# Performance work log

Hardware: AMD Instinct MI355X
Metric: run time of the kernel (lower is better)

The kernel has to match this reference:

```python
import jax, jax.numpy as jnp
import numpy as np

L, B, D = 4096, 4, 1024

def setup_inputs() -> dict:
    key = jax.random.key(0)
    k1, k2, k3, k4 = jax.random.split(key, 4)
    return {
        "x": jax.random.normal(k1, (L, B, D), dtype=jnp.float32),
        "lmlg": jax.random.normal(k2, (D,), dtype=jnp.float32),
        "theta": jax.random.normal(k3, (D,), dtype=jnp.float32),
        "last_conv_init": jax.random.normal(k4, (D,), dtype=jnp.float32),
    }

def reference(x, lmlg, theta, last_conv_init):
    seq_len, batch, dim = x.shape
    # per-channel decay*rotation: c = gamma * e^{i*theta}, gamma = exp(-exp(lmlg))
    gamma = jnp.exp(-jnp.exp(lmlg))                       # [D]
    c = gamma * jnp.exp(1j * theta)                       # [D] complex64
    # causal filter c^n for n = 0..L-1
    n = jnp.arange(seq_len)[:, None]                      # [L,1]
    filt = c[None, :] ** n                                # [L,D] complex64
    # linear (causal) convolution via zero-padded FFT of length 2L
    filt_fft = jnp.fft.fft(filt, n=2 * seq_len, axis=0)   # [2L,D]
    x_fft = jnp.fft.fft(x, n=2 * seq_len, axis=0)         # [2L,B,D]
    conv_filter_x = jnp.fft.ifft(filt_fft[:, None, :] * x_fft, axis=0)[:seq_len]  # [L,B,D]
    # carry-in state (fresh state = last_conv_init expanded; detached in torch)
    last_conv = jax.lax.stop_gradient(
        jnp.broadcast_to(last_conv_init.astype(conv_filter_x.dtype), (batch, dim))
    )                                                     # [B,D]
    conv_with_past = conv_filter_x + last_conv[None, :, :] * filt[:, None, :] * c[None, None, :]
    return conv_with_past.real * x
```

## Files before the change

### kernel.cpp

```cpp
#include <hip/hip_runtime.h>


#define L_  4096
#define B_  4
#define D_  1024
#define BD_ (B_ * D_)

__global__ __launch_bounds__(256) void sc_sum(
    const float* __restrict__ x,
    const float* __restrict__ lmlg,
    const float* __restrict__ theta,
    float2* __restrict__ ws, int ch) {
  const int t  = threadIdx.x;
  const int k  = blockIdx.x / B_;
  const int b  = blockIdx.x % B_;
  const int d0 = t * 4;

  float4 lg = *(const float4*)(lmlg + d0);
  float4 th = *(const float4*)(theta + d0);
  float cr[4], ci[4], sr[4] = {0.f,0.f,0.f,0.f}, si[4] = {0.f,0.f,0.f,0.f};
  {
    float g0 = expf(-expf(lg.x)), g1 = expf(-expf(lg.y));
    float g2 = expf(-expf(lg.z)), g3 = expf(-expf(lg.w));
    cr[0] = g0 * cosf(th.x); ci[0] = g0 * sinf(th.x);
    cr[1] = g1 * cosf(th.y); ci[1] = g1 * sinf(th.y);
    cr[2] = g2 * cosf(th.z); ci[2] = g2 * sinf(th.z);
    cr[3] = g3 * cosf(th.w); ci[3] = g3 * sinf(th.w);
  }

  const float* xp = x + (size_t)k * ch * BD_ + (size_t)b * D_ + d0;
#pragma unroll 4
  for (int j = 0; j < ch; ++j) {
    float4 xv = *(const float4*)(xp + (size_t)j * BD_);
    float xa[4] = {xv.x, xv.y, xv.z, xv.w};
#pragma unroll
    for (int q = 0; q < 4; ++q) {
      float nr = fmaf(cr[q], sr[q], fmaf(-ci[q], si[q], xa[q]));
      float ni = fmaf(cr[q], si[q], ci[q] * sr[q]);
      sr[q] = nr; si[q] = ni;
    }
  }

  float2* wp = ws + (size_t)(k * B_ + b) * D_ + d0;
  wp[0] = make_float2(sr[0], si[0]);
  wp[1] = make_float2(sr[1], si[1]);
  wp[2] = make_float2(sr[2], si[2]);
  wp[3] = make_float2(sr[3], si[3]);
}

__global__ __launch_bounds__(256) void sc_out(
    const float* __restrict__ x,
    const float* __restrict__ lmlg,
    const float* __restrict__ theta,
    const float* __restrict__ init,
    const float2* __restrict__ ws,
    float* __restrict__ out, int ch) {
  const int t  = threadIdx.x;
  const int k  = blockIdx.x / B_;
  const int b  = blockIdx.x % B_;
  const int d0 = t * 4;

  float4 lg = *(const float4*)(lmlg + d0);
  float4 th = *(const float4*)(theta + d0);
  float cr[4], ci[4];
  {
    float g0 = expf(-expf(lg.x)), g1 = expf(-expf(lg.y));
    float g2 = expf(-expf(lg.z)), g3 = expf(-expf(lg.w));
    cr[0] = g0 * cosf(th.x); ci[0] = g0 * sinf(th.x);
    cr[1] = g1 * cosf(th.y); ci[1] = g1 * sinf(th.y);
    cr[2] = g2 * cosf(th.z); ci[2] = g2 * sinf(th.z);
    cr[3] = g3 * cosf(th.w); ci[3] = g3 * sinf(th.w);
  }

  const float chf = (float)ch;
  float Cr[4], Ci[4];
  {
    float e0 = expf(lg.x), e1 = expf(lg.y), e2 = expf(lg.z), e3 = expf(lg.w);
    float g0 = expf(-e0 * chf), g1 = expf(-e1 * chf);
    float g2 = expf(-e2 * chf), g3 = expf(-e3 * chf);
    Cr[0] = g0 * cosf(th.x * chf); Ci[0] = g0 * sinf(th.x * chf);
    Cr[1] = g1 * cosf(th.y * chf); Ci[1] = g1 * sinf(th.y * chf);
    Cr[2] = g2 * cosf(th.z * chf); Ci[2] = g2 * sinf(th.z * chf);
    Cr[3] = g3 * cosf(th.w * chf); Ci[3] = g3 * sinf(th.w * chf);
  }

  float4 iv = *(const float4*)(init + d0);
  float hr[4] = {iv.x, iv.y, iv.z, iv.w};
  float hi[4] = {0.f, 0.f, 0.f, 0.f};
  for (int kk = 0; kk < k; ++kk) {
    const float2* sp = ws + (size_t)(kk * B_ + b) * D_ + d0;
    float2 s0 = sp[0], s1 = sp[1], s2 = sp[2], s3 = sp[3];
    float sxr[4] = {s0.x, s1.x, s2.x, s3.x};
    float sxi[4] = {s0.y, s1.y, s2.y, s3.y};
#pragma unroll
    for (int q = 0; q < 4; ++q) {
      float nr = fmaf(Cr[q], hr[q], fmaf(-Ci[q], hi[q], sxr[q]));
      float ni = fmaf(Cr[q], hi[q], fmaf(Ci[q], hr[q], sxi[q]));
      hr[q] = nr; hi[q] = ni;
    }
  }

  const size_t off = (size_t)k * ch * BD_ + (size_t)b * D_ + d0;
  const float* xp = x + off;
  float*       op = out + off;
#pragma unroll 4
  for (int j = 0; j < ch; ++j) {
    float4 xv = *(const float4*)(xp + (size_t)j * BD_);
    float xa[4] = {xv.x, xv.y, xv.z, xv.w};
    float4 res; float* ra = &res.x;
#pragma unroll
    for (int q = 0; q < 4; ++q) {
      float nr = fmaf(cr[q], hr[q], fmaf(-ci[q], hi[q], xa[q]));
      float ni = fmaf(cr[q], hi[q], ci[q] * hr[q]);
      hr[q] = nr; hi[q] = ni;
      ra[q] = nr * xa[q];
    }
    *(float4*)(op + (size_t)j * BD_) = res;
  }
}

__global__ __launch_bounds__(256) void sc_full(
    const float* __restrict__ x, const float* __restrict__ lmlg,
    const float* __restrict__ theta, const float* __restrict__ init,
    float* __restrict__ out) {
  const int idx = blockIdx.x * 256 + threadIdx.x;
  const int d   = idx & (D_ - 1);
  float g = expf(-expf(lmlg[d]));
  float cr = g * cosf(theta[d]), ci = g * sinf(theta[d]);
  float hr = init[d], hi = 0.f;
  const float* xp = x + idx;
  float*       op = out + idx;
  for (int n = 0; n < L_; ++n) {
    float xv = xp[(size_t)n * BD_];
    float nr = fmaf(cr, hr, fmaf(-ci, hi, xv));
    float ni = fmaf(cr, hi, ci * hr);
    hr = nr; hi = ni;
    op[(size_t)n * BD_] = nr * xv;
  }
}

extern "C" void kernel_launch(void* const* d_in, const int* in_sizes, int n_in,
                              void* d_out, int out_size, void* d_ws, size_t ws_size,
                              hipStream_t stream) {
  const float* x     = (const float*)d_in[0];
  const float* lmlg  = (const float*)d_in[1];
  const float* theta = (const float*)d_in[2];
  const float* init  = (const float*)d_in[3];
  float*  out = (float*)d_out;
  float2* ws  = (float2*)d_ws;

  const size_t row_bytes = (size_t)BD_ * sizeof(float2);
  int nc = 128;
  while (nc > 1 && (size_t)nc * row_bytes > ws_size) nc >>= 1;

  if (nc >= 2 && (size_t)nc * row_bytes <= ws_size) {
    const int ch = L_ / nc;
    sc_sum<<<nc * B_, 256, 0, stream>>>(x, lmlg, theta, ws, ch);
    sc_out<<<nc * B_, 256, 0, stream>>>(x, lmlg, theta, init, ws, out, ch);
  } else {
    sc_full<<<BD_ / 256, 256, 0, stream>>>(x, lmlg, theta, init, out);
  }
}
```

Before: 148.9 us.

## Fuse chunked scan into single decoupled-lookback kernel with register-cached inputs

After: 361.7 us. 2.43x slower.

```diff
diff --git a/kernel.cpp b/kernel.cpp
--- a/kernel.cpp
+++ b/kernel.cpp
@@ -5,117 +5,152 @@
 #define B_  4
 #define D_  1024
 #define BD_ (B_ * D_)
-
-__global__ __launch_bounds__(256) void sc_sum(
-    const float* __restrict__ x,
-    const float* __restrict__ lmlg,
-    const float* __restrict__ theta,
-    float2* __restrict__ ws, int ch) {
-  const int t  = threadIdx.x;
-  const int k  = blockIdx.x / B_;
-  const int b  = blockIdx.x % B_;
-  const int d0 = t * 4;
-
-  float4 lg = *(const float4*)(lmlg + d0);
-  float4 th = *(const float4*)(theta + d0);
-  float cr[4], ci[4], sr[4] = {0.f,0.f,0.f,0.f}, si[4] = {0.f,0.f,0.f,0.f};
-  {
-    float g0 = expf(-expf(lg.x)), g1 = expf(-expf(lg.y));
-    float g2 = expf(-expf(lg.z)), g3 = expf(-expf(lg.w));
-    cr[0] = g0 * cosf(th.x); ci[0] = g0 * sinf(th.x);
-    cr[1] = g1 * cosf(th.y); ci[1] = g1 * sinf(th.y);
-    cr[2] = g2 * cosf(th.z); ci[2] = g2 * sinf(th.z);
-    cr[3] = g3 * cosf(th.w); ci[3] = g3 * sinf(th.w);
-  }
-
-  const float* xp = x + (size_t)k * ch * BD_ + (size_t)b * D_ + d0;
-#pragma unroll 4
-  for (int j = 0; j < ch; ++j) {
-    float4 xv = *(const float4*)(xp + (size_t)j * BD_);
-    float xa[4] = {xv.x, xv.y, xv.z, xv.w};
-#pragma unroll
-    for (int q = 0; q < 4; ++q) {
-      float nr = fmaf(cr[q], sr[q], fmaf(-ci[q], si[q], xa[q]));
-      float ni = fmaf(cr[q], si[q], ci[q] * sr[q]);
-      sr[q] = nr; si[q] = ni;
-    }
-  }
-
-  float2* wp = ws + (size_t)(k * B_ + b) * D_ + d0;
-  wp[0] = make_float2(sr[0], si[0]);
-  wp[1] = make_float2(sr[1], si[1]);
-  wp[2] = make_float2(sr[2], si[2]);
-  wp[3] = make_float2(sr[3], si[3]);
-}
-
-__global__ __launch_bounds__(256) void sc_out(
+#define NC  128
+#define CH  32
+
+
+__global__ __launch_bounds__(256, 2) void sc_lookback(
     const float* __restrict__ x,
     const float* __restrict__ lmlg,
     const float* __restrict__ theta,
     const float* __restrict__ init,
-    const float2* __restrict__ ws,
-    float* __restrict__ out, int ch) {
-  const int t  = threadIdx.x;
-  const int k  = blockIdx.x / B_;
-  const int b  = blockIdx.x % B_;
-  const int d0 = t * 4;
+    float* __restrict__ out,
+    float2* __restrict__ agg,
+    float2* __restrict__ inc,
+    unsigned int* __restrict__ flags) {
+  const int t    = threadIdx.x;
+  const int k    = blockIdx.x / B_;
+  const int b    = blockIdx.x % B_;
+  const int d0   = t * 4;
+  const int lane = t & 63;
 
   float4 lg = *(const float4*)(lmlg + d0);
   float4 th = *(const float4*)(theta + d0);
-  float cr[4], ci[4];
+  float cr[4], ci[4], Cr[4], Ci[4];
   {
-    float g0 = expf(-expf(lg.x)), g1 = expf(-expf(lg.y));
-    float g2 = expf(-expf(lg.z)), g3 = expf(-expf(lg.w));
-    cr[0] = g0 * cosf(th.x); ci[0] = g0 * sinf(th.x);
-    cr[1] = g1 * cosf(th.y); ci[1] = g1 * sinf(th.y);
-    cr[2] = g2 * cosf(th.z); ci[2] = g2 * sinf(th.z);
-    cr[3] = g3 * cosf(th.w); ci[3] = g3 * sinf(th.w);
-  }
-
-  const float chf = (float)ch;
-  float Cr[4], Ci[4];
+    float e[4] = {expf(lg.x), expf(lg.y), expf(lg.z), expf(lg.w)};
+    float ta[4] = {th.x, th.y, th.z, th.w};
+#pragma unroll
+    for (int c = 0; c < 4; ++c) {
+      float g = expf(-e[c]);
+      cr[c] = g * cosf(ta[c]);  ci[c] = g * sinf(ta[c]);
+      float gC = expf(-e[c] * (float)CH);
+      Cr[c] = gC * cosf(ta[c] * (float)CH);
+      Ci[c] = gC * sinf(ta[c] * (float)CH);
+    }
+  }
+
+  const size_t base = (size_t)k * CH * BD_ + (size_t)b * D_ + d0;
+  float4 xv[CH];
+#pragma unroll
+  for (int j = 0; j < CH; ++j)
+    xv[j] = *(const float4*)(x + base + (size_t)j * BD_);
+
+  float sr[4] = {0.f,0.f,0.f,0.f}, si[4] = {0.f,0.f,0.f,0.f};
+#pragma unroll
+  for (int j = 0; j < CH; ++j) {
+    const float* xa = &xv[j].x;
+#pragma unroll
+    for (int c = 0; c < 4; ++c) {
+      float nr = fmaf(cr[c], sr[c], fmaf(-ci[c], si[c], xa[c]));
+      float ni = fmaf(cr[c], si[c], ci[c] * sr[c]);
+      sr[c] = nr; si[c] = ni;
+    }
+  }
+
   {
-    float e0 = expf(lg.x), e1 = expf(lg.y), e2 = expf(lg.z), e3 = expf(lg.w);
-    float g0 = expf(-e0 * chf), g1 = expf(-e1 * chf);
-    float g2 = expf(-e2 * chf), g3 = expf(-e3 * chf);
-    Cr[0] = g0 * cosf(th.x * chf); Ci[0] = g0 * sinf(th.x * chf);
-    Cr[1] = g1 * cosf(th.y * chf); Ci[1] = g1 * sinf(th.y * chf);
-    Cr[2] = g2 * cosf(th.z * chf); Ci[2] = g2 * sinf(th.z * chf);
-    Cr[3] = g3 * cosf(th.w * chf); Ci[3] = g3 * sinf(th.w * chf);
-  }
+    float2* ap = agg + ((size_t)k * B_ + b) * D_ + d0;
+#pragma unroll
+    for (int c = 0; c < 4; ++c) ap[c] = make_float2(sr[c], si[c]);
+  }
+  __threadfence();
+  __syncthreads();
+  if (t == 0)
+    __hip_atomic_store(&flags[k * B_ + b], 1u, __ATOMIC_RELEASE,
+                       __HIP_MEMORY_SCOPE_AGENT);
 
   float4 iv = *(const float4*)(init + d0);
-  float hr[4] = {iv.x, iv.y, iv.z, iv.w};
-  float hi[4] = {0.f, 0.f, 0.f, 0.f};
-  for (int kk = 0; kk < k; ++kk) {
-    const float2* sp = ws + (size_t)(kk * B_ + b) * D_ + d0;
-    float2 s0 = sp[0], s1 = sp[1], s2 = sp[2], s3 = sp[3];
-    float sxr[4] = {s0.x, s1.x, s2.x, s3.x};
-    float sxi[4] = {s0.y, s1.y, s2.y, s3.y};
-#pragma unroll
-    for (int q = 0; q < 4; ++q) {
-      float nr = fmaf(Cr[q], hr[q], fmaf(-Ci[q], hi[q], sxr[q]));
-      float ni = fmaf(Cr[q], hi[q], fmaf(Ci[q], hr[q], sxi[q]));
-      hr[q] = nr; hi[q] = ni;
-    }
-  }
-
-  const size_t off = (size_t)k * ch * BD_ + (size_t)b * D_ + d0;
-  const float* xp = x + off;
-  float*       op = out + off;
-#pragma unroll 4
-  for (int j = 0; j < ch; ++j) {
-    float4 xv = *(const float4*)(xp + (size_t)j * BD_);
-    float xa[4] = {xv.x, xv.y, xv.z, xv.w};
+  float Pr[4] = {iv.x, iv.y, iv.z, iv.w};
+  float Pi[4] = {0.f, 0.f, 0.f, 0.f};
+
+  int jstar = -1;
+  for (int bj = k - 1; bj >= 0; bj -= 64) {
+    int j = bj - lane;
+    unsigned f = 0u;
+    if (j >= 0)
+      f = __hip_atomic_load(&flags[j * B_ + b], __ATOMIC_ACQUIRE,
+                            __HIP_MEMORY_SCOPE_AGENT);
+    unsigned long long m2 = __ballot(j >= 0 && f == 2u);
+    if (m2) { jstar = bj - (__ffsll((unsigned long long)m2) - 1); break; }
+  }
+  if (jstar >= 0) {
+    const float2* ip = inc + ((size_t)jstar * B_ + b) * D_ + d0;
+#pragma unroll
+    for (int c = 0; c < 4; ++c) { float2 h = ip[c]; Pr[c] = h.x; Pi[c] = h.y; }
+  }
+
+  for (int w0 = jstar + 1; w0 < k; w0 += 64) {
+    const int wend = (w0 + 64 < k) ? (w0 + 64) : k;
+    const int idx  = w0 + lane;
+    const bool val = idx < k;
+    unsigned f;
+    unsigned long long m0;
+    do {
+      f = val ? __hip_atomic_load(&flags[idx * B_ + b], __ATOMIC_ACQUIRE,
+                                  __HIP_MEMORY_SCOPE_AGENT)
+              : 1u;
+      m0 = __ballot(f == 0u);
+    } while (m0 != 0ull);
+    unsigned long long m2 = __ballot(val && f == 2u);
+    int q0 = w0;
+    if (m2) {
+      int j2 = w0 + (63 - __clzll(m2));
+      const float2* ip = inc + ((size_t)j2 * B_ + b) * D_ + d0;
+#pragma unroll
+      for (int c = 0; c < 4; ++c) { float2 h = ip[c]; Pr[c] = h.x; Pi[c] = h.y; }
+      q0 = j2 + 1;
+    }
+    for (int q = q0; q < wend; ++q) {
+      const float2* sp = agg + ((size_t)q * B_ + b) * D_ + d0;
+      float2 s0 = sp[0], s1 = sp[1], s2 = sp[2], s3 = sp[3];
+      float sx[4] = {s0.x, s1.x, s2.x, s3.x};
+      float sy[4] = {s0.y, s1.y, s2.y, s3.y};
+#pragma unroll
+      for (int c = 0; c < 4; ++c) {
+        float nr = fmaf(Cr[c], Pr[c], fmaf(-Ci[c], Pi[c], sx[c]));
+        float ni = fmaf(Cr[c], Pi[c], fmaf(Ci[c], Pr[c], sy[c]));
+        Pr[c] = nr; Pi[c] = ni;
+      }
+    }
+  }
+
+  {
+    float2* ip = inc + ((size_t)k * B_ + b) * D_ + d0;
+#pragma unroll
+    for (int c = 0; c < 4; ++c) {
+      float nr = fmaf(Cr[c], Pr[c], fmaf(-Ci[c], Pi[c], sr[c]));
+      float ni = fmaf(Cr[c], Pi[c], fmaf(Ci[c], Pr[c], si[c]));
+      ip[c] = make_float2(nr, ni);
+    }
+  }
+  __threadfence();
+  __syncthreads();
+  if (t == 0)
+    __hip_atomic_store(&flags[k * B_ + b], 2u, __ATOMIC_RELEASE,
+                       __HIP_MEMORY_SCOPE_AGENT);
+
+#pragma unroll
+  for (int j = 0; j < CH; ++j) {
+    const float* xa = &xv[j].x;
     float4 res; float* ra = &res.x;
 #pragma unroll
-    for (int q = 0; q < 4; ++q) {
-      float nr = fmaf(cr[q], hr[q], fmaf(-ci[q], hi[q], xa[q]));
-      float ni = fmaf(cr[q], hi[q], ci[q] * hr[q]);
-      hr[q] = nr; hi[q] = ni;
-      ra[q] = nr * xa[q];
-    }
-    *(float4*)(op + (size_t)j * BD_) = res;
+    for (int c = 0; c < 4; ++c) {
+      float nr = fmaf(cr[c], Pr[c], fmaf(-ci[c], Pi[c], xa[c]));
+      float ni = fmaf(cr[c], Pi[c], ci[c] * Pr[c]);
+      Pr[c] = nr; Pi[c] = ni;
+      ra[c] = nr * xa[c];
+    }
+    *(float4*)(out + base + (size_t)j * BD_) = res;
   }
 }
 
@@ -146,17 +181,19 @@
   const float* lmlg  = (const float*)d_in[1];
   const float* theta = (const float*)d_in[2];
   const float* init  = (const float*)d_in[3];
-  float*  out = (float*)d_out;
-  float2* ws  = (float2*)d_ws;
-
-  const size_t row_bytes = (size_t)BD_ * sizeof(float2);
-  int nc = 128;
-  while (nc > 1 && (size_t)nc * row_bytes > ws_size) nc >>= 1;
-
-  if (nc >= 2 && (size_t)nc * row_bytes <= ws_size) {
-    const int ch = L_ / nc;
-    sc_sum<<<nc * B_, 256, 0, stream>>>(x, lmlg, theta, ws, ch);
-    sc_out<<<nc * B_, 256, 0, stream>>>(x, lmlg, theta, init, ws, out, ch);
+  float* out = (float*)d_out;
+
+  const size_t flag_bytes = 8192;
+  const size_t pay        = (size_t)NC * BD_ * sizeof(float2);
+  const size_t need       = flag_bytes + 2 * pay;
+
+  if (ws_size >= need) {
+    unsigned int* flags = (unsigned int*)d_ws;
+    float2* agg = (float2*)((char*)d_ws + flag_bytes);
+    float2* inc = agg + (size_t)NC * BD_;
+    hipMemsetAsync(flags, 0, NC * B_ * sizeof(unsigned int), stream);
+    sc_lookback<<<NC * B_, 256, 0, stream>>>(x, lmlg, theta, init, out,
+                                             agg, inc, flags);
   } else {
     sc_full<<<BD_ / 256, 256, 0, stream>>>(x, lmlg, theta, init, out);
   }
```
